# Optimization experiments

Measured on AMD Instinct MI355X. Metric: run time of the kernel, lower is better.

The kernel has to match this reference:

```python
import jax, jax.numpy as jnp
import numpy as np

HIDDEN = 2048
N_HEADS = 32
N_KV_HEADS = 8
HEAD_DIM = 64
ROPE_THETA = 500000.0
B, S = 1, 2048


def _rope_tables(seq_len):
    inv_freq = 1.0 / ROPE_THETA ** (jnp.arange(0, HEAD_DIM, 2, dtype=jnp.float32) / HEAD_DIM)
    angles = jnp.arange(seq_len, dtype=jnp.float32)[:, None] * inv_freq[None, :]
    return jnp.cos(angles), jnp.sin(angles)


def _apply_rope(x, cos, sin):
    # x: (B, S, H, D); cos/sin: (S, D//2)
    x1 = x[..., 0::2]
    x2 = x[..., 1::2]
    c = cos[None, :, None, :]
    s = sin[None, :, None, :]
    x1r = x1 * c - x2 * s
    x2r = x1 * s + x2 * c
    return jnp.stack([x1r, x2r], axis=-1).reshape(x.shape)


def setup_inputs() -> dict:
    key = jax.random.key(0)
    ks = jax.random.split(key, 5)
    hidden_states = jax.random.normal(ks[0], (B, S, HIDDEN), dtype=jnp.float32)
    # causal mask, broadcastable over (B, H, S, S)
    attention_mask = jnp.tril(jnp.ones((S, S), dtype=bool))[None, :, :]
    sc = 1.0 / np.sqrt(HIDDEN)
    wq = jax.random.normal(ks[1], (HIDDEN, N_HEADS * HEAD_DIM), dtype=jnp.float32) * sc
    wk = jax.random.normal(ks[2], (HIDDEN, N_KV_HEADS * HEAD_DIM), dtype=jnp.float32) * sc
    wv = jax.random.normal(ks[3], (HIDDEN, N_KV_HEADS * HEAD_DIM), dtype=jnp.float32) * sc
    wo = jax.random.normal(ks[4], (N_HEADS * HEAD_DIM, HIDDEN), dtype=jnp.float32) * sc
    return {"hidden_states": hidden_states, "attention_mask": attention_mask,
            "wq": wq, "wk": wk, "wv": wv, "wo": wo}


def reference(hidden_states, attention_mask, wq, wk, wv, wo):
    b, s, _ = hidden_states.shape
    groups = N_HEADS // N_KV_HEADS
    q = (hidden_states @ wq).reshape(b, s, N_HEADS, HEAD_DIM)
    k = (hidden_states @ wk).reshape(b, s, N_KV_HEADS, HEAD_DIM)
    v = (hidden_states @ wv).reshape(b, s, N_KV_HEADS, HEAD_DIM)
    cos, sin = _rope_tables(s)
    q = _apply_rope(q, cos, sin)
    k = _apply_rope(k, cos, sin)
    k = jnp.repeat(k, groups, axis=2)  # (b, s, H, D)
    v = jnp.repeat(v, groups, axis=2)
    q = q.transpose(0, 2, 1, 3)  # (b, H, s, D)
    k = k.transpose(0, 2, 1, 3)
    v = v.transpose(0, 2, 1, 3)
    scores = jnp.einsum('bhqd,bhkd->bhqk', q, k) / jnp.sqrt(jnp.float32(HEAD_DIM))
    scores = jnp.where(attention_mask[:, None, :, :], scores, -jnp.inf)
    probs = jax.nn.softmax(scores, axis=-1)
    out = jnp.einsum('bhqk,bhkd->bhqd', probs, v)
    out = out.transpose(0, 2, 1, 3).reshape(b, s, N_HEADS * HEAD_DIM)
    return out @ wo
```

## Files before the change

kernel.cpp:

```cpp
#include <hip/hip_runtime.h>

typedef __attribute__((ext_vector_type(8))) short short8;
typedef __attribute__((ext_vector_type(4))) float float4v;

union U4S8 { uint4 u; short8 s; };

__device__ __forceinline__ float bf2f(ushort u) {
    union { uint i; float f; } v; v.i = ((uint)u) << 16; return v.f;
}
__device__ __forceinline__ ushort f2bf(float f) {
    union { uint i; float f; } v; v.f = f;
    return (ushort)((v.i + 0x7FFFu + ((v.i >> 16) & 1u)) >> 16);
}
#if __has_builtin(__builtin_amdgcn_cvt_pk_bf16_f32)
__device__ __forceinline__ uint f2bf_pk(float a, float b) {
    auto r = __builtin_amdgcn_cvt_pk_bf16_f32(a, b);
    return __builtin_bit_cast(uint, r);
}
#else
__device__ __forceinline__ uint f2bf_pk(float a, float b) {
    return (uint)f2bf(a) | ((uint)f2bf(b) << 16);
}
#endif
__device__ __forceinline__ void gld_lds16(const ushort* g, ushort* l) {
    __builtin_amdgcn_global_load_lds((const __attribute__((address_space(1))) unsigned int*)g,
                                     (__attribute__((address_space(3))) unsigned int*)l,
                                     16, 0, 0);
}

__device__ __forceinline__ void tconv_body(const float* in, ushort* out,
                                           int C, int r0, int c0, int tid) {
    __shared__ float t[64][65];
    const int lrow = tid >> 2;
    const int lc   = (tid & 3) * 16;
    const float* ip = in + (size_t)(r0 + lrow) * C + c0 + lc;
#pragma unroll
    for (int i = 0; i < 4; i++) {
        float4 v = *(const float4*)(ip + 4 * i);
        t[lrow][lc + 4 * i + 0] = v.x; t[lrow][lc + 4 * i + 1] = v.y;
        t[lrow][lc + 4 * i + 2] = v.z; t[lrow][lc + 4 * i + 3] = v.w;
    }
    __syncthreads();
    ushort* op = out + (size_t)(c0 + lrow) * 2048 + r0 + lc;
#pragma unroll
    for (int i = 0; i < 8; i++)
        ((uint*)op)[i] = f2bf_pk(t[lc + 2 * i][lrow], t[lc + 2 * i + 1][lrow]);
}

__global__ __launch_bounds__(256) void prep(const float* __restrict__ hidden,
                                            const float* __restrict__ wq,
                                            const float* __restrict__ wk,
                                            const float* __restrict__ wv,
                                            const float* __restrict__ wo,
                                            ushort* __restrict__ hid,
                                            ushort* __restrict__ wT,
                                            ushort* __restrict__ woT) {
    const int bx = blockIdx.x;
    if (bx < 2048) {
        const size_t i = ((size_t)bx * 256 + threadIdx.x) * 8;
        float4 a = *(const float4*)(hidden + i);
        float4 b = *(const float4*)(hidden + i + 4);
        uint4 u;
        u.x = f2bf_pk(a.x, a.y); u.y = f2bf_pk(a.z, a.w);
        u.z = f2bf_pk(b.x, b.y); u.w = f2bf_pk(b.z, b.w);
        *(uint4*)(hid + i) = u;
    } else if (bx < 3584) {
        const int i = bx - 2048;
        const int xx = i % 48, yy = i / 48;
        const float* in; ushort* op; int C, cx;
        if (xx < 32)      { in = wq; op = wT;                        C = 2048; cx = xx; }
        else if (xx < 40) { in = wk; op = wT + (size_t)2048 * 2048;  C = 512;  cx = xx - 32; }
        else              { in = wv; op = wT + (size_t)2560 * 2048;  C = 512;  cx = xx - 40; }
        tconv_body(in, op, C, yy * 64, cx * 64, threadIdx.x);
    } else {
        const int i = bx - 3584;
        tconv_body(wo, woT, 2048, (i >> 5) * 64, (i & 31) * 64, threadIdx.x);
    }
}

template <bool BF16OUT>
__global__ __launch_bounds__(256) void gemm_n64(const ushort* __restrict__ A,
                                                const ushort* __restrict__ Bt,
                                                void* __restrict__ Cout,
                                                int N, int K, int lda, int ropeQKV) {
    __shared__ ushort As[2][128 * 32];
    __shared__ ushort Bs[2][64 * 32];

    const int tid = threadIdx.x, w = tid >> 6, lane = tid & 63;
    const int lr = lane & 15, quad = lane >> 4;
    const int m0 = blockIdx.x * 128, n0 = blockIdx.y * 64;

    const int srow = lane >> 2;
    const int skb  = (lane & 3) ^ ((srow >> 1) & 3);

    const ushort* Ap = A  + (size_t)(m0 + srow) * lda + skb * 8;
    const ushort* Bp = Bt + (size_t)(n0 + w * 16 + srow) * K + skb * 8;

    float4v acc[2][4];
#pragma unroll
    for (int a = 0; a < 2; a++)
#pragma unroll
        for (int b = 0; b < 4; b++) { acc[a][b][0] = 0.f; acc[a][b][1] = 0.f; acc[a][b][2] = 0.f; acc[a][b][3] = 0.f; }

    const int fsw = (lr >> 1) & 3;

#pragma unroll
    for (int i = 0; i < 2; i++) {
        const int rt = 2 * w + i;
        gld_lds16(Ap + (size_t)(rt * 16) * lda, &As[0][rt * 512]);
    }
    gld_lds16(Bp, &Bs[0][w * 512]);

    const int niter = K >> 5;
    for (int it = 0; it < niter; it++) {
        const int b = it & 1;

        asm volatile("s_waitcnt vmcnt(0) lgkmcnt(0)\n\ts_barrier" ::: "memory");

        if (it + 1 < niter) {
            const int k1 = (it + 1) << 5;
#pragma unroll
            for (int i = 0; i < 2; i++) {
                const int rt = 2 * w + i;
                gld_lds16(Ap + (size_t)(rt * 16) * lda + k1, &As[1 - b][rt * 512]);
            }
            gld_lds16(Bp + k1, &Bs[1 - b][w * 512]);
        }

        short8 af[2], bf[4];
#pragma unroll
        for (int mt = 0; mt < 2; mt++)
            af[mt] = *(const short8*)&As[b][(w * 32 + mt * 16 + lr) * 32 + (quad ^ fsw) * 8];
#pragma unroll
        for (int nt = 0; nt < 4; nt++)
            bf[nt] = *(const short8*)&Bs[b][(nt * 16 + lr) * 32 + (quad ^ fsw) * 8];
#pragma unroll
        for (int mt = 0; mt < 2; mt++)
#pragma unroll
            for (int nt = 0; nt < 4; nt++)
                acc[mt][nt] = __builtin_amdgcn_mfma_f32_16x16x32_bf16(af[mt], bf[nt], acc[mt][nt], 0, 0, 0);
    }

    const int rbase = m0 + w * 32 + quad * 4;
    const int cbase = n0 + lr;
    if (BF16OUT) {
        ushort* Cb = (ushort*)Cout;
        if (ropeQKV && (int)blockIdx.y < 40) {
            const float osc = ((int)blockIdx.y < 32) ? 0.18033688f : 1.0f;
            const float sgn = (lr & 1) ? 1.0f : -1.0f;
#pragma unroll
            for (int nt = 0; nt < 4; nt++) {
                const int col = cbase + nt * 16;
                const int j = (col >> 1) & 31;
                const float inv = __expf(-(float)(2 * j) * (1.0f / 64.0f) * 13.122363377404328f);
#pragma unroll
                for (int mt = 0; mt < 2; mt++)
#pragma unroll
                    for (int r = 0; r < 4; r++) {
                        const int row = rbase + mt * 16 + r;
                        float sn, cs;
                        sincosf((float)row * inv, &sn, &cs);
                        const float mine = acc[mt][nt][r];
                        const float partner = __shfl_xor(mine, 1);
                        Cb[(size_t)row * N + col] = f2bf((mine * cs + sgn * partner * sn) * osc);
                    }
            }
        } else {
#pragma unroll
            for (int mt = 0; mt < 2; mt++)
#pragma unroll
                for (int nt = 0; nt < 4; nt++)
#pragma unroll
                    for (int r = 0; r < 4; r++)
                        Cb[(size_t)(rbase + mt * 16 + r) * N + cbase + nt * 16] = f2bf(acc[mt][nt][r]);
        }
    } else {
        float* Cf = (float*)Cout;
#pragma unroll
        for (int mt = 0; mt < 2; mt++)
#pragma unroll
            for (int nt = 0; nt < 4; nt++)
#pragma unroll
                for (int r = 0; r < 4; r++)
                    Cf[(size_t)(rbase + mt * 16 + r) * N + cbase + nt * 16] = acc[mt][nt][r];
    }
}

__global__ __launch_bounds__(256) void attn_mfma(const ushort* __restrict__ Q,
                                                 const ushort* __restrict__ Kc,
                                                 const ushort* __restrict__ Vc,
                                                 ushort* __restrict__ O0,
                                                 ushort* __restrict__ O1,
                                                 float* __restrict__ L0,
                                                 float* __restrict__ L1) {
    __shared__ ushort Ks[2][64 * 64];
    __shared__ ushort Vt[2][64 * 64];
    __shared__ ushort Ps[4][16 * 64];

    const int tid = threadIdx.x, w = tid >> 6, lane = tid & 63;
    const int lr = lane & 15, quad = lane >> 4;
    const int h = blockIdx.y, g = h >> 2, z = blockIdx.z;

    const int dg = tid & 15;
    const int kl = tid >> 4;
    const int ksub = lane >> 3, dsub = lane & 7;
    ushort* Pw = Ps[w];
    ushort* Op = z ? O1 : O0;
    float*  Lp = z ? L1 : L0;

    const ushort* Vp0 = Vc + g * 64 + dg * 4 + (size_t)3072 * kl;
    const ushort* Kp0 = Kc + g * 64 + ((dsub ^ ksub) * 8) + (size_t)3072 * ksub;

    short8 onesf;
#pragma unroll
    for (int j = 0; j < 8; j++) onesf[j] = (short)0x3F80;

    for (int ti = 0; ti < 2; ti++) {
        const int bx = ti ? 31 - (int)blockIdx.x : (int)blockIdx.x;
        const int nch = (bx >= z) ? ((bx - z) >> 1) + 1 : 0;
        const int last = z + 2 * (nch - 1);

        const ushort* qp = Q + (size_t)(bx * 64 + w * 16 + lr) * 3072 + h * 64 + quad * 8;
        const short8 qf0 = *(const short8*)qp;
        const short8 qf1 = *(const short8*)(qp + 32);

        float4v oacc[4], lacc;
#pragma unroll
        for (int t = 0; t < 4; t++) { oacc[t][0] = 0.f; oacc[t][1] = 0.f; oacc[t][2] = 0.f; oacc[t][3] = 0.f; }
        lacc[0] = 0.f; lacc[1] = 0.f; lacc[2] = 0.f; lacc[3] = 0.f;

        uint2 vv[4];
        if (nch) {
#pragma unroll
            for (int t = 0; t < 4; t++)
                vv[t] = *(const uint2*)(Vp0 + (size_t)(z * 64 + 16 * t) * 3072);
        }
        __syncthreads();
        if (nch) {
#pragma unroll
            for (int i = 0; i < 2; i++) {
                const int rt = 2 * w + i;
                gld_lds16(Kp0 + (size_t)(z * 64 + rt * 8) * 3072, &Ks[0][rt * 512]);
            }
        }

        for (int c = 0; c < nch; c++) {
            const int kb = z + 2 * c;
            const int b = c & 1;
            ushort* bKs = Ks[b];
            ushort* bVt = Vt[b];

#pragma unroll
            for (int i = 0; i < 4; i++) {
                const uint sel = (i & 1) ? 0x07060302u : 0x05040100u;
                uint s0 = (i < 2) ? vv[0].x : vv[0].y;
                uint s1 = (i < 2) ? vv[1].x : vv[1].y;
                uint s2 = (i < 2) ? vv[2].x : vv[2].y;
                uint s3 = (i < 2) ? vv[3].x : vv[3].y;
                uint2 pk;
                pk.x = __builtin_amdgcn_perm(s1, s0, sel);
                pk.y = __builtin_amdgcn_perm(s3, s2, sel);
                *(uint2*)&bVt[(dg * 4 + i) * 64 + (kl ^ ((dg & 3) * 4 + i)) * 4] = pk;
            }

            const int kn = (c + 1 < nch) ? kb + 2 : last;
#pragma unroll
            for (int t = 0; t < 4; t++)
                vv[t] = *(const uint2*)(Vp0 + (size_t)(kn * 64 + 16 * t) * 3072);

            asm volatile("s_waitcnt vmcnt(4) lgkmcnt(0)\n\ts_barrier" ::: "memory");

#pragma unroll
            for (int i = 0; i < 2; i++) {
                const int rt = 2 * w + i;
                gld_lds16(Kp0 + (size_t)(kn * 64 + rt * 8) * 3072, &Ks[1 - b][rt * 512]);
            }

            float4v sacc[4];
#pragma unroll
            for (int t = 0; t < 4; t++) { sacc[t][0] = 0.f; sacc[t][1] = 0.f; sacc[t][2] = 0.f; sacc[t][3] = 0.f; }
#pragma unroll
            for (int t = 0; t < 4; t++) {
                const int krow = t * 16 + lr;
                const int sw = lr & 7;
                short8 kf0 = *(const short8*)&bKs[krow * 64 + ((quad)     ^ sw) * 8];
                short8 kf1 = *(const short8*)&bKs[krow * 64 + ((quad + 4) ^ sw) * 8];
                sacc[t] = __builtin_amdgcn_mfma_f32_16x16x32_bf16(qf0, kf0, sacc[t], 0, 0, 0);
                sacc[t] = __builtin_amdgcn_mfma_f32_16x16x32_bf16(qf1, kf1, sacc[t], 0, 0, 0);
            }

            if (kb == bx) {
#pragma unroll
                for (int r = 0; r < 4; r++) {
                    const int qr = w * 16 + quad * 4 + r;
                    float p0 = exp2f(sacc[0][r]), p1 = exp2f(sacc[1][r]);
                    float p2 = exp2f(sacc[2][r]), p3 = exp2f(sacc[3][r]);
                    if (lr > qr)      p0 = 0.f;
                    if (16 + lr > qr) p1 = 0.f;
                    if (32 + lr > qr) p2 = 0.f;
                    if (48 + lr > qr) p3 = 0.f;
                    const int prow = quad * 4 + r;
                    uint2 pk; pk.x = f2bf_pk(p0, p1); pk.y = f2bf_pk(p2, p3);
                    *(uint2*)&Pw[prow * 64 + (lr ^ prow) * 4] = pk;
                }
            } else {
#pragma unroll
                for (int r = 0; r < 4; r++) {
                    const int prow = quad * 4 + r;
                    uint2 pk;
                    pk.x = f2bf_pk(exp2f(sacc[0][r]), exp2f(sacc[1][r]));
                    pk.y = f2bf_pk(exp2f(sacc[2][r]), exp2f(sacc[3][r]));
                    *(uint2*)&Pw[prow * 64 + (lr ^ prow) * 4] = pk;
                }
            }

#pragma unroll
            for (int ks2 = 0; ks2 < 2; ks2++) {
                const int ub = ks2 * 8 + quad * 2;
                U4S8 pu;
                uint2 plo = *(const uint2*)&Pw[lr * 64 + ((ub)     ^ lr) * 4];
                uint2 phi = *(const uint2*)&Pw[lr * 64 + ((ub + 1) ^ lr) * 4];
                pu.u.x = plo.x; pu.u.y = plo.y; pu.u.z = phi.x; pu.u.w = phi.y;
                lacc = __builtin_amdgcn_mfma_f32_16x16x32_bf16(pu.s, onesf, lacc, 0, 0, 0);
#pragma unroll
                for (int t = 0; t < 4; t++) {
                    const int d = t * 16 + lr;
                    U4S8 vu;
                    uint2 vlo = *(const uint2*)&bVt[d * 64 + ((ub)     ^ lr) * 4];
                    uint2 vhi = *(const uint2*)&bVt[d * 64 + ((ub + 1) ^ lr) * 4];
                    vu.u.x = vlo.x; vu.u.y = vlo.y; vu.u.z = vhi.x; vu.u.w = vhi.y;
                    oacc[t] = __builtin_amdgcn_mfma_f32_16x16x32_bf16(pu.s, vu.s, oacc[t], 0, 0, 0);
                }
            }
        }

        ushort* op = Op + (size_t)(bx * 64 + w * 16 + quad * 4) * 2048 + h * 64 + lr;
#pragma unroll
        for (int t = 0; t < 4; t++)
#pragma unroll
            for (int r = 0; r < 4; r++)
                op[(size_t)r * 2048 + t * 16] = f2bf(oacc[t][r]);
        if (lr == 0) {
#pragma unroll
            for (int r = 0; r < 4; r++)
                Lp[h * 2048 + bx * 64 + w * 16 + quad * 4 + r] = lacc[r];
        }
    }
}

__global__ __launch_bounds__(256) void combine(ushort* __restrict__ O0,
                                               const ushort* __restrict__ O1,
                                               const float* __restrict__ L0,
                                               const float* __restrict__ L1) {
    const int idx = blockIdx.x * 256 + threadIdx.x;
    const int r = idx >> 8;
    const int c8 = (idx & 255) * 8;
    const int h = c8 >> 6;
    const float rl = 1.0f / (L0[h * 2048 + r] + L1[h * 2048 + r]);
    uint4 a = *(const uint4*)(O0 + (size_t)r * 2048 + c8);
    uint4 b = *(const uint4*)(O1 + (size_t)r * 2048 + c8);
    uint ua[4] = {a.x, a.y, a.z, a.w}, ub[4] = {b.x, b.y, b.z, b.w};
    uint rr[4];
#pragma unroll
    for (int k = 0; k < 4; k++) {
        float x0 = bf2f((ushort)(ua[k] & 0xFFFFu)) + bf2f((ushort)(ub[k] & 0xFFFFu));
        float x1 = bf2f((ushort)(ua[k] >> 16))     + bf2f((ushort)(ub[k] >> 16));
        rr[k] = f2bf_pk(x0 * rl, x1 * rl);
    }
    uint4 res; res.x = rr[0]; res.y = rr[1]; res.z = rr[2]; res.w = rr[3];
    *(uint4*)(O0 + (size_t)r * 2048 + c8) = res;
}

extern "C" void kernel_launch(void* const* d_in, const int* in_sizes, int n_in,
                              void* d_out, int out_size, void* d_ws, size_t ws_size,
                              hipStream_t stream) {
    const float* hidden = (const float*)d_in[0];
    const float* wq = (const float*)d_in[2];
    const float* wk = (const float*)d_in[3];
    const float* wv = (const float*)d_in[4];
    const float* wo = (const float*)d_in[5];

    ushort* ws = (ushort*)d_ws;
    ushort* hid = ws;
    ushort* wT  = ws + 4194304;
    ushort* woT = ws + 10485760;
    ushort* O1  = wT;
    float*  L0  = (float*)(ws + 8388608);
    float*  L1  = L0 + 65536;
    ushort* QKV = (ushort*)d_out;

    prep<<<4608, 256, 0, stream>>>(hidden, wq, wk, wv, wo, hid, wT, woT);
    gemm_n64<true><<<dim3(16, 48), 256, 0, stream>>>(hid, wT, QKV, 3072, 2048, 2048, 1);
    attn_mfma<<<dim3(16, 32, 2), 256, 0, stream>>>(QKV, QKV + 2048, QKV + 2560,
                                                   hid , O1, L0, L1);
    combine<<<2048, 256, 0, stream>>>(hid, O1, L0, L1);
    gemm_n64<false><<<dim3(16, 32), 256, 0, stream>>>(hid, woT, d_out, 2048, 2048, 2048, 0);
}
```

Baseline: 236.6 us.

## Fuse split-KV combine into output projection GEMM A-tile load

Removes the separate combine kernel and instead merges the two partial attention outputs and normalizes by the summed softmax denominators while loading A tiles inside the output projection GEMM. The aim is to eliminate a kernel launch and a full read/write pass over the attention output buffer. In exchange, A tiles are loaded through registers with per-iteration conversion rather than direct global-to-LDS copies, and both partial buffers are read repeatedly by every column block. The QKV GEMM is de-templated to its bf16 RoPE path only.

```diff
diff --git a/kernel.cpp b/kernel.cpp
--- a/kernel.cpp
+++ b/kernel.cpp
@@ -78,11 +78,10 @@
     }
 }
 
-template <bool BF16OUT>
 __global__ __launch_bounds__(256) void gemm_n64(const ushort* __restrict__ A,
                                                 const ushort* __restrict__ Bt,
-                                                void* __restrict__ Cout,
-                                                int N, int K, int lda, int ropeQKV) {
+                                                ushort* __restrict__ Cb,
+                                                int N, int K, int lda) {
     __shared__ ushort As[2][128 * 32];
     __shared__ ushort Bs[2][64 * 32];
 
@@ -143,47 +142,140 @@
 
     const int rbase = m0 + w * 32 + quad * 4;
     const int cbase = n0 + lr;
-    if (BF16OUT) {
-        ushort* Cb = (ushort*)Cout;
-        if (ropeQKV && (int)blockIdx.y < 40) {
-            const float osc = ((int)blockIdx.y < 32) ? 0.18033688f : 1.0f;
-            const float sgn = (lr & 1) ? 1.0f : -1.0f;
-#pragma unroll
-            for (int nt = 0; nt < 4; nt++) {
-                const int col = cbase + nt * 16;
-                const int j = (col >> 1) & 31;
-                const float inv = __expf(-(float)(2 * j) * (1.0f / 64.0f) * 13.122363377404328f);
-#pragma unroll
-                for (int mt = 0; mt < 2; mt++)
-#pragma unroll
-                    for (int r = 0; r < 4; r++) {
-                        const int row = rbase + mt * 16 + r;
-                        float sn, cs;
-                        sincosf((float)row * inv, &sn, &cs);
-                        const float mine = acc[mt][nt][r];
-                        const float partner = __shfl_xor(mine, 1);
-                        Cb[(size_t)row * N + col] = f2bf((mine * cs + sgn * partner * sn) * osc);
-                    }
-            }
+    if ((int)blockIdx.y < 40) {
+        const float osc = ((int)blockIdx.y < 32) ? 0.18033688f : 1.0f;
+        const float sgn = (lr & 1) ? 1.0f : -1.0f;
+#pragma unroll
+        for (int nt = 0; nt < 4; nt++) {
+            const int col = cbase + nt * 16;
+            const int j = (col >> 1) & 31;
+            const float inv = __expf(-(float)(2 * j) * (1.0f / 64.0f) * 13.122363377404328f);
+#pragma unroll
+            for (int mt = 0; mt < 2; mt++)
+#pragma unroll
+                for (int r = 0; r < 4; r++) {
+                    const int row = rbase + mt * 16 + r;
+                    float sn, cs;
+                    sincosf((float)row * inv, &sn, &cs);
+                    const float mine = acc[mt][nt][r];
+                    const float partner = __shfl_xor(mine, 1);
+                    Cb[(size_t)row * N + col] = f2bf((mine * cs + sgn * partner * sn) * osc);
+                }
+        }
+    } else {
+#pragma unroll
+        for (int mt = 0; mt < 2; mt++)
+#pragma unroll
+            for (int nt = 0; nt < 4; nt++)
+#pragma unroll
+                for (int r = 0; r < 4; r++)
+                    Cb[(size_t)(rbase + mt * 16 + r) * N + cbase + nt * 16] = f2bf(acc[mt][nt][r]);
+    }
+}
+
+__global__ __launch_bounds__(256) void gemm_out(const ushort* __restrict__ O0,
+                                                const ushort* __restrict__ O1,
+                                                const float* __restrict__ L0,
+                                                const float* __restrict__ L1,
+                                                const ushort* __restrict__ Bt,
+                                                float* __restrict__ Cf) {
+    const int N = 2048, K = 2048;
+    __shared__ ushort As[2][128 * 32];
+    __shared__ ushort Bs[2][64 * 32];
+
+    const int tid = threadIdx.x, w = tid >> 6, lane = tid & 63;
+    const int lr = lane & 15, quad = lane >> 4;
+    const int m0 = blockIdx.x * 128, n0 = blockIdx.y * 64;
+
+    const int srow = lane >> 2;
+    const int skb  = (lane & 3) ^ ((srow >> 1) & 3);
+
+    const int rowA = m0 + 2 * w * 16 + srow;
+    const int rowB = rowA + 16;
+    const ushort* Bp = Bt + (size_t)(n0 + w * 16 + srow) * K + skb * 8;
+
+    float4v acc[2][4];
+#pragma unroll
+    for (int a = 0; a < 2; a++)
+#pragma unroll
+        for (int b = 0; b < 4; b++) { acc[a][b][0] = 0.f; acc[a][b][1] = 0.f; acc[a][b][2] = 0.f; acc[a][b][3] = 0.f; }
+
+    const int fsw = (lr >> 1) & 3;
+
+    uint4 oa0 = *(const uint4*)(O0 + (size_t)rowA * 2048 + skb * 8);
+    uint4 oa1 = *(const uint4*)(O1 + (size_t)rowA * 2048 + skb * 8);
+    uint4 ob0 = *(const uint4*)(O0 + (size_t)rowB * 2048 + skb * 8);
+    uint4 ob1 = *(const uint4*)(O1 + (size_t)rowB * 2048 + skb * 8);
+    float l0a = L0[rowA], l1a = L1[rowA];
+    float l0b = L0[rowB], l1b = L1[rowB];
+    gld_lds16(Bp, &Bs[0][w * 512]);
+
+    const int niter = K >> 5;
+    for (int it = 0; it < niter; it++) {
+        const int b = it & 1;
+
+        {
+            const float rla = 1.0f / (l0a + l1a);
+            const float rlb = 1.0f / (l0b + l1b);
+            uint ua[4] = {oa0.x, oa0.y, oa0.z, oa0.w};
+            uint va[4] = {oa1.x, oa1.y, oa1.z, oa1.w};
+            uint ub[4] = {ob0.x, ob0.y, ob0.z, ob0.w};
+            uint vb[4] = {ob1.x, ob1.y, ob1.z, ob1.w};
+            uint4 ra, rb;
+            uint rra[4], rrb[4];
+#pragma unroll
+            for (int k = 0; k < 4; k++) {
+                float lo = (bf2f((ushort)(ua[k] & 0xFFFFu)) + bf2f((ushort)(va[k] & 0xFFFFu))) * rla;
+                float hi = (bf2f((ushort)(ua[k] >> 16))     + bf2f((ushort)(va[k] >> 16)))     * rla;
+                rra[k] = f2bf_pk(lo, hi);
+                float lo2 = (bf2f((ushort)(ub[k] & 0xFFFFu)) + bf2f((ushort)(vb[k] & 0xFFFFu))) * rlb;
+                float hi2 = (bf2f((ushort)(ub[k] >> 16))     + bf2f((ushort)(vb[k] >> 16)))     * rlb;
+                rrb[k] = f2bf_pk(lo2, hi2);
+            }
+            ra.x = rra[0]; ra.y = rra[1]; ra.z = rra[2]; ra.w = rra[3];
+            rb.x = rrb[0]; rb.y = rrb[1]; rb.z = rrb[2]; rb.w = rrb[3];
+            *(uint4*)&As[b][(2 * w)     * 512 + srow * 32 + (lane & 3) * 8] = ra;
+            *(uint4*)&As[b][(2 * w + 1) * 512 + srow * 32 + (lane & 3) * 8] = rb;
+        }
+
+        if (it + 1 < niter) {
+            const int kk = (it + 1) * 32 + skb * 8;
+            const int h2 = (it + 1) >> 1;
+            oa0 = *(const uint4*)(O0 + (size_t)rowA * 2048 + kk);
+            oa1 = *(const uint4*)(O1 + (size_t)rowA * 2048 + kk);
+            ob0 = *(const uint4*)(O0 + (size_t)rowB * 2048 + kk);
+            ob1 = *(const uint4*)(O1 + (size_t)rowB * 2048 + kk);
+            l0a = L0[h2 * 2048 + rowA]; l1a = L1[h2 * 2048 + rowA];
+            l0b = L0[h2 * 2048 + rowB]; l1b = L1[h2 * 2048 + rowB];
+            asm volatile("s_waitcnt vmcnt(8) lgkmcnt(0)\n\ts_barrier" ::: "memory");
+            gld_lds16(Bp + (it + 1) * 32, &Bs[1 - b][w * 512]);
         } else {
-#pragma unroll
-            for (int mt = 0; mt < 2; mt++)
-#pragma unroll
-                for (int nt = 0; nt < 4; nt++)
-#pragma unroll
-                    for (int r = 0; r < 4; r++)
-                        Cb[(size_t)(rbase + mt * 16 + r) * N + cbase + nt * 16] = f2bf(acc[mt][nt][r]);
-        }
-    } else {
-        float* Cf = (float*)Cout;
+            asm volatile("s_waitcnt vmcnt(0) lgkmcnt(0)\n\ts_barrier" ::: "memory");
+        }
+
+        short8 af[2], bf[4];
 #pragma unroll
         for (int mt = 0; mt < 2; mt++)
+            af[mt] = *(const short8*)&As[b][(w * 32 + mt * 16 + lr) * 32 + (quad ^ fsw) * 8];
+#pragma unroll
+        for (int nt = 0; nt < 4; nt++)
+            bf[nt] = *(const short8*)&Bs[b][(nt * 16 + lr) * 32 + (quad ^ fsw) * 8];
+#pragma unroll
+        for (int mt = 0; mt < 2; mt++)
 #pragma unroll
             for (int nt = 0; nt < 4; nt++)
-#pragma unroll
-                for (int r = 0; r < 4; r++)
-                    Cf[(size_t)(rbase + mt * 16 + r) * N + cbase + nt * 16] = acc[mt][nt][r];
-    }
+                acc[mt][nt] = __builtin_amdgcn_mfma_f32_16x16x32_bf16(af[mt], bf[nt], acc[mt][nt], 0, 0, 0);
+    }
+
+    const int rbase = m0 + w * 32 + quad * 4;
+    const int cbase = n0 + lr;
+#pragma unroll
+    for (int mt = 0; mt < 2; mt++)
+#pragma unroll
+        for (int nt = 0; nt < 4; nt++)
+#pragma unroll
+            for (int r = 0; r < 4; r++)
+                Cf[(size_t)(rbase + mt * 16 + r) * N + cbase + nt * 16] = acc[mt][nt][r];
 }
 
 __global__ __launch_bounds__(256) void attn_mfma(const ushort* __restrict__ Q,
@@ -348,29 +440,6 @@
     }
 }
 
-__global__ __launch_bounds__(256) void combine(ushort* __restrict__ O0,
-                                               const ushort* __restrict__ O1,
-                                               const float* __restrict__ L0,
-                                               const float* __restrict__ L1) {
-    const int idx = blockIdx.x * 256 + threadIdx.x;
-    const int r = idx >> 8;
-    const int c8 = (idx & 255) * 8;
-    const int h = c8 >> 6;
-    const float rl = 1.0f / (L0[h * 2048 + r] + L1[h * 2048 + r]);
-    uint4 a = *(const uint4*)(O0 + (size_t)r * 2048 + c8);
-    uint4 b = *(const uint4*)(O1 + (size_t)r * 2048 + c8);
-    uint ua[4] = {a.x, a.y, a.z, a.w}, ub[4] = {b.x, b.y, b.z, b.w};
-    uint rr[4];
-#pragma unroll
-    for (int k = 0; k < 4; k++) {
-        float x0 = bf2f((ushort)(ua[k] & 0xFFFFu)) + bf2f((ushort)(ub[k] & 0xFFFFu));
-        float x1 = bf2f((ushort)(ua[k] >> 16))     + bf2f((ushort)(ub[k] >> 16));
-        rr[k] = f2bf_pk(x0 * rl, x1 * rl);
-    }
-    uint4 res; res.x = rr[0]; res.y = rr[1]; res.z = rr[2]; res.w = rr[3];
-    *(uint4*)(O0 + (size_t)r * 2048 + c8) = res;
-}
-
 extern "C" void kernel_launch(void* const* d_in, const int* in_sizes, int n_in,
                               void* d_out, int out_size, void* d_ws, size_t ws_size,
                               hipStream_t stream) {
@@ -390,9 +459,8 @@
     ushort* QKV = (ushort*)d_out;
 
     prep<<<4608, 256, 0, stream>>>(hidden, wq, wk, wv, wo, hid, wT, woT);
-    gemm_n64<true><<<dim3(16, 48), 256, 0, stream>>>(hid, wT, QKV, 3072, 2048, 2048, 1);
+    gemm_n64<<<dim3(16, 48), 256, 0, stream>>>(hid, wT, QKV, 3072, 2048, 2048);
     attn_mfma<<<dim3(16, 32, 2), 256, 0, stream>>>(QKV, QKV + 2048, QKV + 2560,
                                                    hid , O1, L0, L1);
-    combine<<<2048, 256, 0, stream>>>(hid, O1, L0, L1);
-    gemm_n64<false><<<dim3(16, 32), 256, 0, stream>>>(hid, woT, d_out, 2048, 2048, 2048, 0);
-}
+    gemm_out<<<dim3(16, 32), 256, 0, stream>>>(hid, O1, L0, L1, woT, (float*)d_out);
+}
```

Measured after the change: 261.4 us. 10.5% more time.

## Drop split-K attention, assign one query tile per block and fuse normalization

Applied to the files above, without the earlier changes.

Before, each block handled two query tiles, one from each end of the causal range, for a balanced load, and the KV range was split across z into two halves that a separate combine kernel merged. Now each block handles one query tile over the full KV range, using z to select the mirrored tile, and divides by the row sum in the epilogue. This removes the combine kernel launch, the partial O and L writes, and their re-reads. In exchange each block's causal work is unbalanced: late tiles loop up to 32 KV chunks, which lengthens the critical path. Grid size is unchanged.

```diff
diff --git a/kernel.cpp b/kernel.cpp
--- a/kernel.cpp
+++ b/kernel.cpp
@@ -189,24 +189,20 @@
 __global__ __launch_bounds__(256) void attn_mfma(const ushort* __restrict__ Q,
                                                  const ushort* __restrict__ Kc,
                                                  const ushort* __restrict__ Vc,
-                                                 ushort* __restrict__ O0,
-                                                 ushort* __restrict__ O1,
-                                                 float* __restrict__ L0,
-                                                 float* __restrict__ L1) {
+                                                 ushort* __restrict__ Ab) {
     __shared__ ushort Ks[2][64 * 64];
     __shared__ ushort Vt[2][64 * 64];
     __shared__ ushort Ps[4][16 * 64];
 
     const int tid = threadIdx.x, w = tid >> 6, lane = tid & 63;
     const int lr = lane & 15, quad = lane >> 4;
-    const int h = blockIdx.y, g = h >> 2, z = blockIdx.z;
+    const int h = blockIdx.y, g = h >> 2;
+    const int bx = blockIdx.z ? 31 - (int)blockIdx.x : (int)blockIdx.x;
 
     const int dg = tid & 15;
     const int kl = tid >> 4;
     const int ksub = lane >> 3, dsub = lane & 7;
     ushort* Pw = Ps[w];
-    ushort* Op = z ? O1 : O0;
-    float*  Lp = z ? L1 : L0;
 
     const ushort* Vp0 = Vc + g * 64 + dg * 4 + (size_t)3072 * kl;
     const ushort* Kp0 = Kc + g * 64 + ((dsub ^ ksub) * 8) + (size_t)3072 * ksub;
@@ -215,160 +211,120 @@
 #pragma unroll
     for (int j = 0; j < 8; j++) onesf[j] = (short)0x3F80;
 
-    for (int ti = 0; ti < 2; ti++) {
-        const int bx = ti ? 31 - (int)blockIdx.x : (int)blockIdx.x;
-        const int nch = (bx >= z) ? ((bx - z) >> 1) + 1 : 0;
-        const int last = z + 2 * (nch - 1);
-
-        const ushort* qp = Q + (size_t)(bx * 64 + w * 16 + lr) * 3072 + h * 64 + quad * 8;
-        const short8 qf0 = *(const short8*)qp;
-        const short8 qf1 = *(const short8*)(qp + 32);
-
-        float4v oacc[4], lacc;
-#pragma unroll
-        for (int t = 0; t < 4; t++) { oacc[t][0] = 0.f; oacc[t][1] = 0.f; oacc[t][2] = 0.f; oacc[t][3] = 0.f; }
-        lacc[0] = 0.f; lacc[1] = 0.f; lacc[2] = 0.f; lacc[3] = 0.f;
-
-        uint2 vv[4];
-        if (nch) {
-#pragma unroll
-            for (int t = 0; t < 4; t++)
-                vv[t] = *(const uint2*)(Vp0 + (size_t)(z * 64 + 16 * t) * 3072);
-        }
-        __syncthreads();
-        if (nch) {
-#pragma unroll
-            for (int i = 0; i < 2; i++) {
-                const int rt = 2 * w + i;
-                gld_lds16(Kp0 + (size_t)(z * 64 + rt * 8) * 3072, &Ks[0][rt * 512]);
-            }
-        }
-
-        for (int c = 0; c < nch; c++) {
-            const int kb = z + 2 * c;
-            const int b = c & 1;
-            ushort* bKs = Ks[b];
-            ushort* bVt = Vt[b];
-
-#pragma unroll
-            for (int i = 0; i < 4; i++) {
-                const uint sel = (i & 1) ? 0x07060302u : 0x05040100u;
-                uint s0 = (i < 2) ? vv[0].x : vv[0].y;
-                uint s1 = (i < 2) ? vv[1].x : vv[1].y;
-                uint s2 = (i < 2) ? vv[2].x : vv[2].y;
-                uint s3 = (i < 2) ? vv[3].x : vv[3].y;
+    const ushort* qp = Q + (size_t)(bx * 64 + w * 16 + lr) * 3072 + h * 64 + quad * 8;
+    const short8 qf0 = *(const short8*)qp;
+    const short8 qf1 = *(const short8*)(qp + 32);
+
+    float4v oacc[4], lacc;
+#pragma unroll
+    for (int t = 0; t < 4; t++) { oacc[t][0] = 0.f; oacc[t][1] = 0.f; oacc[t][2] = 0.f; oacc[t][3] = 0.f; }
+    lacc[0] = 0.f; lacc[1] = 0.f; lacc[2] = 0.f; lacc[3] = 0.f;
+
+    uint2 vv[4];
+#pragma unroll
+    for (int t = 0; t < 4; t++)
+        vv[t] = *(const uint2*)(Vp0 + (size_t)(16 * t) * 3072);
+#pragma unroll
+    for (int i = 0; i < 2; i++) {
+        const int rt = 2 * w + i;
+        gld_lds16(Kp0 + (size_t)(rt * 8) * 3072, &Ks[0][rt * 512]);
+    }
+
+    for (int kb = 0; kb <= bx; kb++) {
+        const int b = kb & 1;
+        ushort* bKs = Ks[b];
+        ushort* bVt = Vt[b];
+
+#pragma unroll
+        for (int i = 0; i < 4; i++) {
+            const uint sel = (i & 1) ? 0x07060302u : 0x05040100u;
+            uint s0 = (i < 2) ? vv[0].x : vv[0].y;
+            uint s1 = (i < 2) ? vv[1].x : vv[1].y;
+            uint s2 = (i < 2) ? vv[2].x : vv[2].y;
+            uint s3 = (i < 2) ? vv[3].x : vv[3].y;
+            uint2 pk;
+            pk.x = __builtin_amdgcn_perm(s1, s0, sel);
+            pk.y = __builtin_amdgcn_perm(s3, s2, sel);
+            *(uint2*)&bVt[(dg * 4 + i) * 64 + (kl ^ ((dg & 3) * 4 + i)) * 4] = pk;
+        }
+
+        const int kn = (kb < bx) ? kb + 1 : bx;
+#pragma unroll
+        for (int t = 0; t < 4; t++)
+            vv[t] = *(const uint2*)(Vp0 + (size_t)(kn * 64 + 16 * t) * 3072);
+
+        asm volatile("s_waitcnt vmcnt(4) lgkmcnt(0)\n\ts_barrier" ::: "memory");
+
+#pragma unroll
+        for (int i = 0; i < 2; i++) {
+            const int rt = 2 * w + i;
+            gld_lds16(Kp0 + (size_t)(kn * 64 + rt * 8) * 3072, &Ks[1 - b][rt * 512]);
+        }
+
+        float4v sacc[4];
+#pragma unroll
+        for (int t = 0; t < 4; t++) { sacc[t][0] = 0.f; sacc[t][1] = 0.f; sacc[t][2] = 0.f; sacc[t][3] = 0.f; }
+#pragma unroll
+        for (int t = 0; t < 4; t++) {
+            const int krow = t * 16 + lr;
+            const int sw = lr & 7;
+            short8 kf0 = *(const short8*)&bKs[krow * 64 + ((quad)     ^ sw) * 8];
+            short8 kf1 = *(const short8*)&bKs[krow * 64 + ((quad + 4) ^ sw) * 8];
+            sacc[t] = __builtin_amdgcn_mfma_f32_16x16x32_bf16(qf0, kf0, sacc[t], 0, 0, 0);
+            sacc[t] = __builtin_amdgcn_mfma_f32_16x16x32_bf16(qf1, kf1, sacc[t], 0, 0, 0);
+        }
+
+        if (kb == bx) {
+#pragma unroll
+            for (int r = 0; r < 4; r++) {
+                const int qr = w * 16 + quad * 4 + r;
+                float p0 = exp2f(sacc[0][r]), p1 = exp2f(sacc[1][r]);
+                float p2 = exp2f(sacc[2][r]), p3 = exp2f(sacc[3][r]);
+                if (lr > qr)      p0 = 0.f;
+                if (16 + lr > qr) p1 = 0.f;
+                if (32 + lr > qr) p2 = 0.f;
+                if (48 + lr > qr) p3 = 0.f;
+                const int prow = quad * 4 + r;
+                uint2 pk; pk.x = f2bf_pk(p0, p1); pk.y = f2bf_pk(p2, p3);
+                *(uint2*)&Pw[prow * 64 + (lr ^ prow) * 4] = pk;
+            }
+        } else {
+#pragma unroll
+            for (int r = 0; r < 4; r++) {
+                const int prow = quad * 4 + r;
                 uint2 pk;
-                pk.x = __builtin_amdgcn_perm(s1, s0, sel);
-                pk.y = __builtin_amdgcn_perm(s3, s2, sel);
-                *(uint2*)&bVt[(dg * 4 + i) * 64 + (kl ^ ((dg & 3) * 4 + i)) * 4] = pk;
-            }
-
-            const int kn = (c + 1 < nch) ? kb + 2 : last;
-#pragma unroll
-            for (int t = 0; t < 4; t++)
-                vv[t] = *(const uint2*)(Vp0 + (size_t)(kn * 64 + 16 * t) * 3072);
-
-            asm volatile("s_waitcnt vmcnt(4) lgkmcnt(0)\n\ts_barrier" ::: "memory");
-
-#pragma unroll
-            for (int i = 0; i < 2; i++) {
-                const int rt = 2 * w + i;
-                gld_lds16(Kp0 + (size_t)(kn * 64 + rt * 8) * 3072, &Ks[1 - b][rt * 512]);
-            }
-
-            float4v sacc[4];
-#pragma unroll
-            for (int t = 0; t < 4; t++) { sacc[t][0] = 0.f; sacc[t][1] = 0.f; sacc[t][2] = 0.f; sacc[t][3] = 0.f; }
+                pk.x = f2bf_pk(exp2f(sacc[0][r]), exp2f(sacc[1][r]));
+                pk.y = f2bf_pk(exp2f(sacc[2][r]), exp2f(sacc[3][r]));
+                *(uint2*)&Pw[prow * 64 + (lr ^ prow) * 4] = pk;
+            }
+        }
+
+#pragma unroll
+        for (int ks2 = 0; ks2 < 2; ks2++) {
+            const int ub = ks2 * 8 + quad * 2;
+            U4S8 pu;
+            uint2 plo = *(const uint2*)&Pw[lr * 64 + ((ub)     ^ lr) * 4];
+            uint2 phi = *(const uint2*)&Pw[lr * 64 + ((ub + 1) ^ lr) * 4];
+            pu.u.x = plo.x; pu.u.y = plo.y; pu.u.z = phi.x; pu.u.w = phi.y;
+            lacc = __builtin_amdgcn_mfma_f32_16x16x32_bf16(pu.s, onesf, lacc, 0, 0, 0);
 #pragma unroll
             for (int t = 0; t < 4; t++) {
-                const int krow = t * 16 + lr;
-                const int sw = lr & 7;
-                short8 kf0 = *(const short8*)&bKs[krow * 64 + ((quad)     ^ sw) * 8];
-                short8 kf1 = *(const short8*)&bKs[krow * 64 + ((quad + 4) ^ sw) * 8];
-                sacc[t] = __builtin_amdgcn_mfma_f32_16x16x32_bf16(qf0, kf0, sacc[t], 0, 0, 0);
-                sacc[t] = __builtin_amdgcn_mfma_f32_16x16x32_bf16(qf1, kf1, sacc[t], 0, 0, 0);
-            }
-
-            if (kb == bx) {
-#pragma unroll
-                for (int r = 0; r < 4; r++) {
-                    const int qr = w * 16 + quad * 4 + r;
-                    float p0 = exp2f(sacc[0][r]), p1 = exp2f(sacc[1][r]);
-                    float p2 = exp2f(sacc[2][r]), p3 = exp2f(sacc[3][r]);
-                    if (lr > qr)      p0 = 0.f;
-                    if (16 + lr > qr) p1 = 0.f;
-                    if (32 + lr > qr) p2 = 0.f;
-                    if (48 + lr > qr) p3 = 0.f;
-                    const int prow = quad * 4 + r;
-                    uint2 pk; pk.x = f2bf_pk(p0, p1); pk.y = f2bf_pk(p2, p3);
-                    *(uint2*)&Pw[prow * 64 + (lr ^ prow) * 4] = pk;
-                }
-            } else {
-#pragma unroll
-                for (int r = 0; r < 4; r++) {
-                    const int prow = quad * 4 + r;
-                    uint2 pk;
-                    pk.x = f2bf_pk(exp2f(sacc[0][r]), exp2f(sacc[1][r]));
-                    pk.y = f2bf_pk(exp2f(sacc[2][r]), exp2f(sacc[3][r]));
-                    *(uint2*)&Pw[prow * 64 + (lr ^ prow) * 4] = pk;
-                }
-            }
-
-#pragma unroll
-            for (int ks2 = 0; ks2 < 2; ks2++) {
-                const int ub = ks2 * 8 + quad * 2;
-                U4S8 pu;
-                uint2 plo = *(const uint2*)&Pw[lr * 64 + ((ub)     ^ lr) * 4];
-                uint2 phi = *(const uint2*)&Pw[lr * 64 + ((ub + 1) ^ lr) * 4];
-                pu.u.x = plo.x; pu.u.y = plo.y; pu.u.z = phi.x; pu.u.w = phi.y;
-                lacc = __builtin_amdgcn_mfma_f32_16x16x32_bf16(pu.s, onesf, lacc, 0, 0, 0);
-#pragma unroll
-                for (int t = 0; t < 4; t++) {
-                    const int d = t * 16 + lr;
-                    U4S8 vu;
-                    uint2 vlo = *(const uint2*)&bVt[d * 64 + ((ub)     ^ lr) * 4];
-                    uint2 vhi = *(const uint2*)&bVt[d * 64 + ((ub + 1) ^ lr) * 4];
-                    vu.u.x = vlo.x; vu.u.y = vlo.y; vu.u.z = vhi.x; vu.u.w = vhi.y;
-                    oacc[t] = __builtin_amdgcn_mfma_f32_16x16x32_bf16(pu.s, vu.s, oacc[t], 0, 0, 0);
-                }
-            }
-        }
-
-        ushort* op = Op + (size_t)(bx * 64 + w * 16 + quad * 4) * 2048 + h * 64 + lr;
-#pragma unroll
-        for (int t = 0; t < 4; t++)
-#pragma unroll
-            for (int r = 0; r < 4; r++)
-                op[(size_t)r * 2048 + t * 16] = f2bf(oacc[t][r]);
-        if (lr == 0) {
-#pragma unroll
-            for (int r = 0; r < 4; r++)
-                Lp[h * 2048 + bx * 64 + w * 16 + quad * 4 + r] = lacc[r];
-        }
-    }
-}
-
-__global__ __launch_bounds__(256) void combine(ushort* __restrict__ O0,
-                                               const ushort* __restrict__ O1,
-                                               const float* __restrict__ L0,
-                                               const float* __restrict__ L1) {
-    const int idx = blockIdx.x * 256 + threadIdx.x;
-    const int r = idx >> 8;
-    const int c8 = (idx & 255) * 8;
-    const int h = c8 >> 6;
-    const float rl = 1.0f / (L0[h * 2048 + r] + L1[h * 2048 + r]);
-    uint4 a = *(const uint4*)(O0 + (size_t)r * 2048 + c8);
-    uint4 b = *(const uint4*)(O1 + (size_t)r * 2048 + c8);
-    uint ua[4] = {a.x, a.y, a.z, a.w}, ub[4] = {b.x, b.y, b.z, b.w};
-    uint rr[4];
-#pragma unroll
-    for (int k = 0; k < 4; k++) {
-        float x0 = bf2f((ushort)(ua[k] & 0xFFFFu)) + bf2f((ushort)(ub[k] & 0xFFFFu));
-        float x1 = bf2f((ushort)(ua[k] >> 16))     + bf2f((ushort)(ub[k] >> 16));
-        rr[k] = f2bf_pk(x0 * rl, x1 * rl);
-    }
-    uint4 res; res.x = rr[0]; res.y = rr[1]; res.z = rr[2]; res.w = rr[3];
-    *(uint4*)(O0 + (size_t)r * 2048 + c8) = res;
+                const int d = t * 16 + lr;
+                U4S8 vu;
+                uint2 vlo = *(const uint2*)&bVt[d * 64 + ((ub)     ^ lr) * 4];
+                uint2 vhi = *(const uint2*)&bVt[d * 64 + ((ub + 1) ^ lr) * 4];
+                vu.u.x = vlo.x; vu.u.y = vlo.y; vu.u.z = vhi.x; vu.u.w = vhi.y;
+                oacc[t] = __builtin_amdgcn_mfma_f32_16x16x32_bf16(pu.s, vu.s, oacc[t], 0, 0, 0);
+            }
+        }
+    }
+
+    ushort* op = Ab + (size_t)(bx * 64 + w * 16 + quad * 4) * 2048 + h * 64 + lr;
+#pragma unroll
+    for (int t = 0; t < 4; t++)
+#pragma unroll
+        for (int r = 0; r < 4; r++)
+            op[(size_t)r * 2048 + t * 16] = f2bf(oacc[t][r] / lacc[r]);
 }
 
 extern "C" void kernel_launch(void* const* d_in, const int* in_sizes, int n_in,
@@ -384,15 +340,10 @@
     ushort* hid = ws;
     ushort* wT  = ws + 4194304;
     ushort* woT = ws + 10485760;
-    ushort* O1  = wT;
-    float*  L0  = (float*)(ws + 8388608);
-    float*  L1  = L0 + 65536;
     ushort* QKV = (ushort*)d_out;
 
     prep<<<4608, 256, 0, stream>>>(hidden, wq, wk, wv, wo, hid, wT, woT);
     gemm_n64<true><<<dim3(16, 48), 256, 0, stream>>>(hid, wT, QKV, 3072, 2048, 2048, 1);
-    attn_mfma<<<dim3(16, 32, 2), 256, 0, stream>>>(QKV, QKV + 2048, QKV + 2560,
-                                                   hid , O1, L0, L1);
-    combine<<<2048, 256, 0, stream>>>(hid, O1, L0, L1);
+    attn_mfma<<<dim3(16, 32, 2), 256, 0, stream>>>(QKV, QKV + 2048, QKV + 2560, hid);
     gemm_n64<false><<<dim3(16, 32), 256, 0, stream>>>(hid, woT, d_out, 2048, 2048, 2048, 0);
 }
```

Measured after the change: 248.1 us. +4.9%, slower.
